# Optimization experiments

Measured on AMD Instinct MI355X. Metric: run time of the kernel, lower is better.

Reference implementation:

```python
import jax, jax.numpy as jnp
import numpy as np

EMBED = 768
HEADS = 6
HEAD_DIM = 256
SEQ = 128
BATCH = 512
EPS = 1e-5


def _layernorm(x, g, b):
    mu = jnp.mean(x, axis=-1, keepdims=True)
    var = jnp.mean(jnp.square(x - mu), axis=-1, keepdims=True)
    return (x - mu) * jax.lax.rsqrt(var + EPS) * g + b


def setup_inputs() -> dict:
    key = jax.random.key(0)
    ks = jax.random.split(key, 10)
    s_in = 1.0 / np.sqrt(EMBED)
    s_cat = 1.0 / np.sqrt(HEADS * HEAD_DIM)
    s_ff = 1.0 / np.sqrt(4 * EMBED)
    return {
        "x": jax.random.normal(ks[0], (BATCH, SEQ, EMBED), jnp.float32),
        # per-head projections (bias=False), stacked over heads: [H, E, D]
        "Wq": jax.random.uniform(ks[1], (HEADS, EMBED, HEAD_DIM), jnp.float32, -s_in, s_in),
        "Wk": jax.random.uniform(ks[2], (HEADS, EMBED, HEAD_DIM), jnp.float32, -s_in, s_in),
        "Wv": jax.random.uniform(ks[3], (HEADS, EMBED, HEAD_DIM), jnp.float32, -s_in, s_in),
        "Wo": jax.random.uniform(ks[4], (HEADS * HEAD_DIM, EMBED), jnp.float32, -s_cat, s_cat),
        "bo": jax.random.uniform(ks[5], (EMBED,), jnp.float32, -s_cat, s_cat),
        "W1": jax.random.uniform(ks[6], (EMBED, 4 * EMBED), jnp.float32, -s_in, s_in),
        "b1": jax.random.uniform(ks[7], (4 * EMBED,), jnp.float32, -s_in, s_in),
        "W2": jax.random.uniform(ks[8], (4 * EMBED, EMBED), jnp.float32, -s_ff, s_ff),
        "b2": jax.random.uniform(ks[9], (EMBED,), jnp.float32, -s_ff, s_ff),
        "g1": jnp.ones((EMBED,), jnp.float32),
        "be1": jnp.zeros((EMBED,), jnp.float32),
        "g2": jnp.ones((EMBED,), jnp.float32),
        "be2": jnp.zeros((EMBED,), jnp.float32),
    }


def reference(x, Wq, Wk, Wv, Wo, bo, W1, b1, W2, b2, g1, be1, g2, be2):
    B, T, E = x.shape
    h = _layernorm(x, g1, be1)
    # per-head projections: [B, H, T, D]
    q = jnp.einsum("bte,hed->bhtd", h, Wq)
    k = jnp.einsum("bte,hed->bhtd", h, Wk)
    v = jnp.einsum("bte,hed->bhtd", h, Wv)
    # NOTE: faithful to source — scale by embed_size**-0.5, not head_size**-0.5
    scores = jnp.einsum("bhtd,bhsd->bhts", q, k) * (E ** -0.5)
    causal = jnp.tril(jnp.ones((T, T), bool))
    scores = jnp.where(causal, scores, -jnp.inf)
    attn = jax.nn.softmax(scores, axis=-1)
    head_out = jnp.einsum("bhts,bhsd->bhtd", attn, v)
    # concat heads in order -> [B, T, H*D]
    cat = head_out.transpose(0, 2, 1, 3).reshape(B, T, HEADS * HEAD_DIM)
    attn_out = cat @ Wo + bo + x
    h2 = _layernorm(attn_out, g2, be2)
    mlp = jax.nn.relu(h2 @ W1 + b1) @ W2 + b2
    return mlp + attn_out
```

## Files before the change

kernel.cpp:

```cpp
#include <hip/hip_runtime.h>
#include <hip/hip_bf16.h>

#define BATCH 512
#define SEQ   128
#define EMB   768
#define NH    6
#define HDIM  256
#define CATD  1536
#define FFD   3072
#define NTOK  (BATCH*SEQ)
#define QKVLD 4608

typedef __attribute__((ext_vector_type(8))) short bfrag;
typedef __attribute__((ext_vector_type(4))) float f32x4;

__device__ __forceinline__ void gld_lds16(const void* g, void* l) {
  __builtin_amdgcn_global_load_lds(
      (const __attribute__((address_space(1))) unsigned int*)g,
      (__attribute__((address_space(3))) unsigned int*)l, 16, 0, 0);
}

__device__ __forceinline__ unsigned short f2bfu(float f) {
  union { __hip_bfloat16 h; unsigned short u; } c;
  c.h = __float2bfloat16(f);
  return c.u;
}

__device__ __forceinline__ void transpose64(const float* in, int C,
                                            __hip_bfloat16* out, int R,
                                            int r0, int c0) {
  __shared__ float tile[64][65];
  const int tx = threadIdx.x & 63;
  const int ty = threadIdx.x >> 6;
#pragma unroll
  for (int i = 0; i < 16; ++i) {
    const int r = ty + i * 4;
    tile[r][tx] = in[(size_t)(r0 + r) * C + c0 + tx];
  }
  __syncthreads();
#pragma unroll
  for (int i = 0; i < 16; ++i) {
    const int cc = ty + i * 4;
    out[(size_t)(c0 + cc) * R + r0 + tx] = __float2bfloat16(tile[tx][cc]);
  }
}

__global__ __launch_bounds__(256) void transpose_cast(const float* __restrict__ in,
                                                      __hip_bfloat16* __restrict__ out,
                                                      int R, int C) {
  transpose64(in, C, out, R, blockIdx.y * 64, blockIdx.x * 64);
}

__global__ __launch_bounds__(256) void repack_qkv(const float* __restrict__ Wq,
                                                  const float* __restrict__ Wk,
                                                  const float* __restrict__ Wv,
                                                  __hip_bfloat16* __restrict__ out) {
  const int z = blockIdx.z, m = z / NH, h = z % NH;
  const float* in = (m == 0 ? Wq : (m == 1 ? Wk : Wv)) + (size_t)h * EMB * HDIM;
  __hip_bfloat16* o = out + (size_t)(m * CATD + h * HDIM) * EMB;
  transpose64(in, HDIM, o, EMB, blockIdx.y * 64, blockIdx.x * 64);
}

__global__ __launch_bounds__(256) void ln_k(const float* __restrict__ src,
                                            const float* __restrict__ gam,
                                            const float* __restrict__ bet,
                                            __hip_bfloat16* __restrict__ dst) {
  const int row = blockIdx.x * 4 + (threadIdx.x >> 6);
  const int l = threadIdx.x & 63;
  const float* x = src + (size_t)row * EMB;
  float4 v[3];
#pragma unroll
  for (int j = 0; j < 3; ++j) v[j] = *(const float4*)(x + j * 256 + l * 4);
  float s = 0.f, ss = 0.f;
#pragma unroll
  for (int j = 0; j < 3; ++j) {
    s  += v[j].x + v[j].y + v[j].z + v[j].w;
    ss += v[j].x * v[j].x + v[j].y * v[j].y + v[j].z * v[j].z + v[j].w * v[j].w;
  }
#pragma unroll
  for (int d = 1; d < 64; d <<= 1) { s += __shfl_xor(s, d, 64); ss += __shfl_xor(ss, d, 64); }
  const float mu = s * (1.f / EMB);
  const float var = ss * (1.f / EMB) - mu * mu;
  const float rs = rsqrtf(var + 1e-5f);
#pragma unroll
  for (int j = 0; j < 3; ++j) {
    float4 g4 = *(const float4*)(gam + j * 256 + l * 4);
    float4 b4 = *(const float4*)(bet + j * 256 + l * 4);
    ushort4 o;
    o.x = f2bfu((v[j].x - mu) * rs * g4.x + b4.x);
    o.y = f2bfu((v[j].y - mu) * rs * g4.y + b4.y);
    o.z = f2bfu((v[j].z - mu) * rs * g4.z + b4.z);
    o.w = f2bfu((v[j].w - mu) * rs * g4.w + b4.w);
    *(ushort4*)((unsigned short*)dst + (size_t)row * EMB + j * 256 + l * 4) = o;
  }
}

#define PHASE(S, MH) do {                                                    \
    bfrag af[4], bv[4];                                                      \
    const char* Ab = cbuf + ((S)*16 + wm*8 + (MH)*4) * 1024 + l * 16;        \
    const char* Bb = cbuf + 32768 + ((S)*16 + wn*4) * 1024 + l * 16;         \
    _Pragma("unroll")                                                        \
    for (int i = 0; i < 4; ++i) af[i] = *(const bfrag*)(Ab + i * 1024);      \
    _Pragma("unroll")                                                        \
    for (int n = 0; n < 4; ++n) bv[n] = *(const bfrag*)(Bb + n * 1024);      \
    __builtin_amdgcn_s_setprio(1);                                          \
    _Pragma("unroll")                                                        \
    for (int i = 0; i < 4; ++i)                                              \
      _Pragma("unroll")                                                      \
      for (int n = 0; n < 4; ++n)                                            \
        acc[(MH)*4 + i][n] = __builtin_amdgcn_mfma_f32_16x16x32_bf16(        \
            af[i], bv[n], acc[(MH)*4 + i][n], 0, 0, 0);                      \
    __builtin_amdgcn_s_setprio(0);                                          \
  } while (0)

#define PH_END                                                \
  asm volatile("s_waitcnt lgkmcnt(0)" ::: "memory");          \
  asm volatile("s_barrier" ::: "memory")

#define STG(p, koff, dstoff) gld_lds16((p) + (koff), lds + (dstoff))

template <int MODE>
__global__ __launch_bounds__(512, 2)
void gemm_k(const __hip_bfloat16* __restrict__ A, const __hip_bfloat16* __restrict__ Bt,
            void* __restrict__ Cout, const float* __restrict__ bias,
            const float* __restrict__ res, int M, int N, int K) {
  __shared__ char lds[131072];
  const int tid = threadIdx.x;
  const int w = tid >> 6, l = tid & 63;
  const int l15 = l & 15, lq = l >> 4;
  const int wm = w >> 2, wn = w & 3;

  const int nwg = gridDim.x * gridDim.y;
  const int orig = blockIdx.y * gridDim.x + blockIdx.x;
  const int cpx = nwg >> 3;
  const int sw = (orig & 7) * cpx + (orig >> 3);
  const int n0 = (sw % gridDim.x) * 256;
  const int m0 = (sw / gridDim.x) * 256;

  const unsigned short* Au = (const unsigned short*)A;
  const unsigned short* Bu = (const unsigned short*)Bt;
  const unsigned short* pA_lo = Au + (size_t)(m0 + w * 16 + l15) * K + lq * 8;
  const unsigned short* pA_hi = Au + (size_t)(m0 + 128 + w * 16 + l15) * K + lq * 8;
  const unsigned short* pB_lo = Bu + (size_t)(n0 + w * 16 + l15) * K + lq * 8;
  const unsigned short* pB_hi = Bu + (size_t)(n0 + 128 + w * 16 + l15) * K + lq * 8;

  f32x4 acc[8][4];
#pragma unroll
  for (int i = 0; i < 8; ++i)
#pragma unroll
    for (int n = 0; n < 4; ++n) acc[i][n] = {0.f, 0.f, 0.f, 0.f};

  const int kIters = K >> 6;

  STG(pA_lo, 0,  (0 + w) * 1024);
  STG(pA_hi, 0,  (8 + w) * 1024);
  STG(pB_lo, 0,  32768 + (0 + w) * 1024);
  STG(pB_hi, 0,  32768 + (8 + w) * 1024);
  STG(pA_lo, 32, (16 + w) * 1024);
  STG(pA_hi, 32, (24 + w) * 1024);
  STG(pB_lo, 32, 32768 + (16 + w) * 1024);
  STG(pB_hi, 32, 32768 + (24 + w) * 1024);
  STG(pA_lo, 64, 65536 + (0 + w) * 1024);
  STG(pA_hi, 64, 65536 + (8 + w) * 1024);
  STG(pB_lo, 64, 65536 + 32768 + (0 + w) * 1024);
  STG(pB_hi, 64, 65536 + 32768 + (8 + w) * 1024);

  for (int kt = 0; kt < kIters; ++kt) {
    const int cOff = (kt & 1) * 65536;
    const int nOff = cOff ^ 65536;
    const char* cbuf = lds + cOff;
    const bool pre1 = (kt + 1 < kIters);
    const bool pre2 = (kt + 2 < kIters);
    const int k1 = (kt + 1) * 64 + 32;
    const int k2 = (kt + 2) * 64;

    if (pre1) {
      STG(pA_lo, k1, nOff + (16 + w) * 1024);
      STG(pB_lo, k1, nOff + 32768 + (16 + w) * 1024);
      asm volatile("s_waitcnt vmcnt(6)" ::: "memory");
    } else {
      asm volatile("s_waitcnt vmcnt(0)" ::: "memory");
    }
    asm volatile("s_barrier" ::: "memory");
    PHASE(0, 0);
    PH_END;
    if (pre1) {
      STG(pA_hi, k1, nOff + (24 + w) * 1024);
      STG(pB_hi, k1, nOff + 32768 + (24 + w) * 1024);
    }
    PHASE(0, 1);
    PH_END;
    if (pre2) {
      STG(pA_lo, k2, cOff + (0 + w) * 1024);
      STG(pB_lo, k2, cOff + 32768 + (0 + w) * 1024);
    }
    PHASE(1, 0);
    PH_END;
    if (pre2) {
      STG(pA_hi, k2, cOff + (8 + w) * 1024);
      STG(pB_hi, k2, cOff + 32768 + (8 + w) * 1024);
    }
    PHASE(1, 1);
    PH_END;
  }

  float bcol[4];
  if (MODE != 0) {
#pragma unroll
    for (int n = 0; n < 4; ++n) bcol[n] = bias[n0 + wn * 64 + n * 16 + l15];
  }
  if (MODE == 1) {
#pragma unroll
    for (int q = 0; q < 4; ++q) {
      if (q) __syncthreads();
      if (wm == (q >> 1)) {
#pragma unroll
        for (int i2 = 0; i2 < 4; ++i2)
#pragma unroll
          for (int n = 0; n < 4; ++n)
#pragma unroll
            for (int r = 0; r < 4; ++r) {
              const int lrow = i2 * 16 + lq * 4 + r;
              const int col = wn * 64 + n * 16 + l15;
              ((float*)lds)[lrow * 260 + col] = acc[(q & 1) * 4 + i2][n][r] + bcol[n];
            }
      }
      __syncthreads();
#pragma unroll
      for (int rep = 0; rep < 8; ++rep) {
        const int row = rep * 8 + (tid >> 6);
        const int colf = (tid & 63) * 4;
        float4 v = *(const float4*)((const float*)lds + row * 260 + colf);
        const size_t gidx = (size_t)(m0 + q * 64 + row) * N + n0 + colf;
        const float4 rv = *(const float4*)(res + gidx);
        v.x += rv.x; v.y += rv.y; v.z += rv.z; v.w += rv.w;
        *(float4*)((float*)Cout + gidx) = v;
      }
    }
  } else {
#pragma unroll
    for (int p = 0; p < 2; ++p) {
      if (p) __syncthreads();
      if (wm == p) {
#pragma unroll
        for (int i = 0; i < 8; ++i)
#pragma unroll
          for (int n = 0; n < 4; ++n)
#pragma unroll
            for (int r = 0; r < 4; ++r) {
              const int lrow = i * 16 + lq * 4 + r;
              const int col = wn * 64 + n * 16 + l15;
              float v = acc[i][n][r];
              if (MODE == 2) v = fmaxf(v + bcol[n], 0.f);
              ((unsigned short*)lds)[lrow * 264 + col] = f2bfu(v);
            }
      }
      __syncthreads();
#pragma unroll
      for (int rep = 0; rep < 8; ++rep) {
        const int row = rep * 16 + (tid >> 5);
        const int colc = (tid & 31) * 8;
        const uint4 v = *(const uint4*)((const unsigned short*)lds + row * 264 + colc);
        *(uint4*)((__hip_bfloat16*)Cout + (size_t)(m0 + p * 128 + row) * N + n0 + colc) = v;
      }
    }
  }
}

#undef PHASE
#undef PH_END
#undef STG

__global__ __launch_bounds__(256, 2)
void attn_k(const __hip_bfloat16* __restrict__ qkv, __hip_bfloat16* __restrict__ cat) {
  __shared__ char sm[17408 + 34816 + 2048];
  char* stage = sm;
  unsigned short* P = (unsigned short*)(sm + 17408);
  float* redm = (float*)(sm + 17408 + 34816);
  float* reds = redm + 256;

  const int tid = threadIdx.x;
  const int w = tid >> 6, l = tid & 63;
  const int l15 = l & 15, lq = l >> 4;
  const int wm = w >> 1, wn = w & 1;
  const int bh = blockIdx.x, b = bh / NH, h = bh % NH;
  const unsigned short* qkvu = (const unsigned short*)qkv;
  const size_t tokbase = (size_t)b * SEQ;
  const int qcol = h * HDIM, kcol = CATD + h * HDIM, vcol = 2 * CATD + h * HDIM;

  f32x4 acc[4][4];
#pragma unroll
  for (int i = 0; i < 4; ++i)
#pragma unroll
    for (int j = 0; j < 4; ++j) acc[i][j] = {0.f, 0.f, 0.f, 0.f};

  for (int d0 = 0; d0 < HDIM; d0 += 32) {
#pragma unroll
    for (int i = 0; i < 4; ++i) {
      const int ch = w * 4 + i;
      const int rowloc = (ch & 7) * 16 + l15;
      const int colbase = (ch < 8 ? qcol : kcol) + d0 + lq * 8;
      gld_lds16(qkvu + (tokbase + rowloc) * QKVLD + colbase, stage + ch * 1024);
    }
    __syncthreads();
    bfrag af[4], bf[4];
#pragma unroll
    for (int i = 0; i < 4; ++i) {
      af[i] = *(const bfrag*)(stage + ((wm * 4 + i) * 64 + l) * 16);
      bf[i] = *(const bfrag*)(stage + 8192 + ((wn * 4 + i) * 64 + l) * 16);
    }
#pragma unroll
    for (int i = 0; i < 4; ++i)
#pragma unroll
      for (int j = 0; j < 4; ++j)
        acc[i][j] = __builtin_amdgcn_mfma_f32_16x16x32_bf16(af[i], bf[j], acc[i][j], 0, 0, 0);
    __syncthreads();
  }

  const float scl = 0.03608439182435161f;
  const int rowb = wm * 64 + lq * 4;
  const int colb = wn * 64 + l15;
  float rmax[4][4];
#pragma unroll
  for (int i = 0; i < 4; ++i)
#pragma unroll
    for (int r = 0; r < 4; ++r) {
      const int row = rowb + i * 16 + r;
      float m = -__builtin_inff();
#pragma unroll
      for (int j = 0; j < 4; ++j) {
        const int col = colb + j * 16;
        float sv = acc[i][j][r] * scl;
        if (col > row) sv = -__builtin_inff();
        acc[i][j][r] = sv;
        m = fmaxf(m, sv);
      }
#pragma unroll
      for (int d = 1; d < 16; d <<= 1) m = fmaxf(m, __shfl_xor(m, d, 64));
      rmax[i][r] = m;
    }
  if (l15 == 0) {
#pragma unroll
    for (int i = 0; i < 4; ++i)
#pragma unroll
      for (int r = 0; r < 4; ++r)
        redm[wn * 128 + rowb + i * 16 + r] = rmax[i][r];
  }
  __syncthreads();
  float rsum[4][4];
#pragma unroll
  for (int i = 0; i < 4; ++i)
#pragma unroll
    for (int r = 0; r < 4; ++r) {
      const int row = rowb + i * 16 + r;
      const float mfin = fmaxf(redm[row], redm[128 + row]);
      float sacc = 0.f;
#pragma unroll
      for (int j = 0; j < 4; ++j) {
        float p = __expf(acc[i][j][r] - mfin);
        acc[i][j][r] = p;
        sacc += p;
      }
#pragma unroll
      for (int d = 1; d < 16; d <<= 1) sacc += __shfl_xor(sacc, d, 64);
      rsum[i][r] = sacc;
    }
  if (l15 == 0) {
#pragma unroll
    for (int i = 0; i < 4; ++i)
#pragma unroll
      for (int r = 0; r < 4; ++r)
        reds[wn * 128 + rowb + i * 16 + r] = rsum[i][r];
  }
#pragma unroll
  for (int i = 0; i < 4; ++i)
#pragma unroll
    for (int j = 0; j < 4; ++j)
#pragma unroll
      for (int r = 0; r < 4; ++r)
        P[(rowb + i * 16 + r) * 136 + colb + j * 16] = f2bfu(acc[i][j][r]);
  __syncthreads();

  float invs[4][4];
#pragma unroll
  for (int i = 0; i < 4; ++i)
#pragma unroll
    for (int r = 0; r < 4; ++r) {
      const int row = rowb + i * 16 + r;
      invs[i][r] = 1.f / (reds[row] + reds[128 + row]);
    }

  unsigned short* Vt = (unsigned short*)stage;
  for (int dt = 0; dt < 4; ++dt) {
#pragma unroll
    for (int p4 = 0; p4 < 4; ++p4) {
      const int slot = tid + p4 * 256;
      const int s = slot >> 3, dblk = slot & 7;
      uint4 val = *(const uint4*)(qkvu + (tokbase + s) * QKVLD + vcol + dt * 64 + dblk * 8);
      union { uint4 v; unsigned short u[8]; } uu; uu.v = val;
#pragma unroll
      for (int jj = 0; jj < 8; ++jj) Vt[(dblk * 8 + jj) * 136 + s] = uu.u[jj];
    }
    __syncthreads();
    f32x4 oacc[4][2];
#pragma unroll
    for (int i = 0; i < 4; ++i) { oacc[i][0] = {0.f,0.f,0.f,0.f}; oacc[i][1] = {0.f,0.f,0.f,0.f}; }
#pragma unroll
    for (int ks = 0; ks < 4; ++ks) {
      bfrag pf[4], vf[2];
#pragma unroll
      for (int i = 0; i < 4; ++i)
        pf[i] = *(const bfrag*)((char*)P + ((wm * 64 + i * 16 + l15) * 136 + ks * 32 + lq * 8) * 2);
#pragma unroll
      for (int j = 0; j < 2; ++j)
        vf[j] = *(const bfrag*)((char*)Vt + (((wn * 2 + j) * 16 + l15) * 136 + ks * 32 + lq * 8) * 2);
#pragma unroll
      for (int i = 0; i < 4; ++i)
#pragma unroll
        for (int j = 0; j < 2; ++j)
          oacc[i][j] = __builtin_amdgcn_mfma_f32_16x16x32_bf16(pf[i], vf[j], oacc[i][j], 0, 0, 0);
    }
#pragma unroll
    for (int i = 0; i < 4; ++i)
#pragma unroll
      for (int j = 0; j < 2; ++j)
#pragma unroll
        for (int r = 0; r < 4; ++r) {
          const int trow = rowb + i * 16 + r;
          const int dcol = dt * 64 + wn * 32 + j * 16 + l15;
          cat[(tokbase + trow) * CATD + h * HDIM + dcol] =
              __float2bfloat16(oacc[i][j][r] * invs[i][r]);
        }
    __syncthreads();
  }
}

extern "C" void kernel_launch(void* const* d_in, const int* in_sizes, int n_in,
                              void* d_out, int out_size, void* d_ws, size_t ws_size,
                              hipStream_t stream) {
  const float* x   = (const float*)d_in[0];
  const float* Wq  = (const float*)d_in[1];
  const float* Wk  = (const float*)d_in[2];
  const float* Wv  = (const float*)d_in[3];
  const float* Wo  = (const float*)d_in[4];
  const float* bo  = (const float*)d_in[5];
  const float* W1  = (const float*)d_in[6];
  const float* b1  = (const float*)d_in[7];
  const float* W2  = (const float*)d_in[8];
  const float* b2  = (const float*)d_in[9];
  const float* g1  = (const float*)d_in[10];
  const float* be1 = (const float*)d_in[11];
  const float* g2  = (const float*)d_in[12];
  const float* be2 = (const float*)d_in[13];
  float* out = (float*)d_out;

  const size_t wbytes = (size_t)QKVLD * EMB * 2 + (size_t)EMB * CATD * 2 +
                        (size_t)FFD * EMB * 2 + (size_t)EMB * FFD * 2;
  int nc = 1;
  while (nc < 16 &&
         wbytes + (size_t)(NTOK / nc) * (9216 + 3072 + 3072) + 4096 > ws_size)
    nc <<= 1;
  const int Mc = NTOK / nc;
  const int Bc = BATCH / nc;

  char* ws = (char*)d_ws;
  size_t off = 0;
  auto alloc = [&](size_t bytes) {
    char* p = ws + off;
    off += (bytes + 255) & ~(size_t)255;
    return p;
  };
  __hip_bfloat16* Wqkv_t = (__hip_bfloat16*)alloc((size_t)QKVLD * EMB * 2);
  __hip_bfloat16* Wo_t   = (__hip_bfloat16*)alloc((size_t)EMB * CATD * 2);
  __hip_bfloat16* W1_t   = (__hip_bfloat16*)alloc((size_t)FFD * EMB * 2);
  __hip_bfloat16* W2_t   = (__hip_bfloat16*)alloc((size_t)EMB * FFD * 2);
  char* R1 = (char*)alloc((size_t)Mc * 9216);
  char* R2 = (char*)alloc((size_t)Mc * 3072);
  char* R3 = (char*)alloc((size_t)Mc * 3072);

  repack_qkv<<<dim3(HDIM / 64, EMB / 64, 18), 256, 0, stream>>>(Wq, Wk, Wv, Wqkv_t);
  transpose_cast<<<dim3(EMB / 64, CATD / 64), 256, 0, stream>>>(Wo, Wo_t, CATD, EMB);
  transpose_cast<<<dim3(FFD / 64, EMB / 64), 256, 0, stream>>>(W1, W1_t, EMB, FFD);
  transpose_cast<<<dim3(EMB / 64, FFD / 64), 256, 0, stream>>>(W2, W2_t, FFD, EMB);

  for (int c = 0; c < nc; ++c) {
    const float* xc   = x + (size_t)c * Mc * EMB;
    float*       outc = out + (size_t)c * Mc * EMB;
    __hip_bfloat16* hbuf   = (__hip_bfloat16*)R3;
    __hip_bfloat16* qkv    = (__hip_bfloat16*)R1;
    __hip_bfloat16* cat    = (__hip_bfloat16*)R2;
    float*          attn_o = (float*)R3;
    __hip_bfloat16* h2     = (__hip_bfloat16*)R2;
    __hip_bfloat16* mlp1   = (__hip_bfloat16*)R1;

    ln_k<<<Mc / 4, 256, 0, stream>>>(xc, g1, be1, hbuf);
    gemm_k<0><<<dim3(QKVLD / 256, Mc / 256), 512, 0, stream>>>(
        hbuf, Wqkv_t, qkv, nullptr, nullptr, Mc, QKVLD, EMB);
    attn_k<<<Bc * NH, 256, 0, stream>>>(qkv, cat);
    gemm_k<1><<<dim3(EMB / 256, Mc / 256), 512, 0, stream>>>(
        cat, Wo_t, attn_o, bo, xc, Mc, EMB, CATD);
    ln_k<<<Mc / 4, 256, 0, stream>>>(attn_o, g2, be2, h2);
    gemm_k<2><<<dim3(FFD / 256, Mc / 256), 512, 0, stream>>>(
        h2, W1_t, mlp1, b1, nullptr, Mc, FFD, EMB);
    gemm_k<1><<<dim3(EMB / 256, Mc / 256), 512, 0, stream>>>(
        mlp1, W2_t, outc, b2, attn_o, Mc, EMB, FFD);
  }
}
```

Measured before the change: 2.429 ms.

## Reorder GEMM main loop to issue LDS reads before global prefetch

Each GEMM phase is split into an LDS fragment-read step and an MFMA step. The LDS reads are now issued before the next global-to-LDS prefetch, and barriers wrap the MFMA block. The vmcnt wait moves from the start of each k-iteration to its last phase, with a new wait and barrier after the prologue. The aim is to overlap LDS read latency with the global load issue and to tighten the synchronisation schedule, at the cost of one extra barrier per phase.

Result: no change. 2.384 ms (-1.8%).

```diff
diff --git a/kernel.cpp b/kernel.cpp
--- a/kernel.cpp
+++ b/kernel.cpp
@@ -95,27 +95,29 @@
   }
 }
 
-#define PHASE(S, MH) do {                                                    \
+#define PH_DS(S, MH)                                                         \
     bfrag af[4], bv[4];                                                      \
-    const char* Ab = cbuf + ((S)*16 + wm*8 + (MH)*4) * 1024 + l * 16;        \
-    const char* Bb = cbuf + 32768 + ((S)*16 + wn*4) * 1024 + l * 16;         \
-    _Pragma("unroll")                                                        \
-    for (int i = 0; i < 4; ++i) af[i] = *(const bfrag*)(Ab + i * 1024);      \
-    _Pragma("unroll")                                                        \
-    for (int n = 0; n < 4; ++n) bv[n] = *(const bfrag*)(Bb + n * 1024);      \
-    __builtin_amdgcn_s_setprio(1);                                          \
+    {                                                                        \
+      const char* Ab = cbuf + ((S)*16 + wm*8 + (MH)*4) * 1024 + l * 16;      \
+      const char* Bb = cbuf + 32768 + ((S)*16 + wn*4) * 1024 + l * 16;       \
+      _Pragma("unroll")                                                      \
+      for (int i = 0; i < 4; ++i) af[i] = *(const bfrag*)(Ab + i * 1024);    \
+      _Pragma("unroll")                                                      \
+      for (int n = 0; n < 4; ++n) bv[n] = *(const bfrag*)(Bb + n * 1024);    \
+    }
+
+#define PH_MFMA(MH)                                                          \
+    __builtin_amdgcn_s_barrier();                                            \
+    asm volatile("s_waitcnt lgkmcnt(0)" ::: "memory");                       \
+    __builtin_amdgcn_s_setprio(1);                                           \
     _Pragma("unroll")                                                        \
     for (int i = 0; i < 4; ++i)                                              \
       _Pragma("unroll")                                                      \
       for (int n = 0; n < 4; ++n)                                            \
         acc[(MH)*4 + i][n] = __builtin_amdgcn_mfma_f32_16x16x32_bf16(        \
             af[i], bv[n], acc[(MH)*4 + i][n], 0, 0, 0);                      \
-    __builtin_amdgcn_s_setprio(0);                                          \
-  } while (0)
-
-#define PH_END                                                \
-  asm volatile("s_waitcnt lgkmcnt(0)" ::: "memory");          \
-  asm volatile("s_barrier" ::: "memory")
+    __builtin_amdgcn_s_setprio(0);                                           \
+    __builtin_amdgcn_s_barrier();
 
 #define STG(p, koff, dstoff) gld_lds16((p) + (koff), lds + (dstoff))
 
@@ -164,6 +166,8 @@
   STG(pA_hi, 64, 65536 + (8 + w) * 1024);
   STG(pB_lo, 64, 65536 + 32768 + (0 + w) * 1024);
   STG(pB_hi, 64, 65536 + 32768 + (8 + w) * 1024);
+  asm volatile("s_waitcnt vmcnt(4)" ::: "memory");
+  __builtin_amdgcn_s_barrier();
 
   for (int kt = 0; kt < kIters; ++kt) {
     const int cOff = (kt & 1) * 65536;
@@ -174,34 +178,41 @@
     const int k1 = (kt + 1) * 64 + 32;
     const int k2 = (kt + 2) * 64;
 
-    if (pre1) {
-      STG(pA_lo, k1, nOff + (16 + w) * 1024);
-      STG(pB_lo, k1, nOff + 32768 + (16 + w) * 1024);
-      asm volatile("s_waitcnt vmcnt(6)" ::: "memory");
-    } else {
-      asm volatile("s_waitcnt vmcnt(0)" ::: "memory");
-    }
-    asm volatile("s_barrier" ::: "memory");
-    PHASE(0, 0);
-    PH_END;
-    if (pre1) {
-      STG(pA_hi, k1, nOff + (24 + w) * 1024);
-      STG(pB_hi, k1, nOff + 32768 + (24 + w) * 1024);
-    }
-    PHASE(0, 1);
-    PH_END;
-    if (pre2) {
-      STG(pA_lo, k2, cOff + (0 + w) * 1024);
-      STG(pB_lo, k2, cOff + 32768 + (0 + w) * 1024);
-    }
-    PHASE(1, 0);
-    PH_END;
-    if (pre2) {
-      STG(pA_hi, k2, cOff + (8 + w) * 1024);
-      STG(pB_hi, k2, cOff + 32768 + (8 + w) * 1024);
-    }
-    PHASE(1, 1);
-    PH_END;
+    {
+      PH_DS(0, 0);
+      if (pre1) {
+        STG(pA_lo, k1, nOff + (16 + w) * 1024);
+        STG(pB_lo, k1, nOff + 32768 + (16 + w) * 1024);
+      }
+      PH_MFMA(0);
+    }
+    {
+      PH_DS(0, 1);
+      if (pre1) {
+        STG(pA_hi, k1, nOff + (24 + w) * 1024);
+        STG(pB_hi, k1, nOff + 32768 + (24 + w) * 1024);
+      }
+      PH_MFMA(1);
+    }
+    {
+      PH_DS(1, 0);
+      if (pre2) {
+        STG(pA_lo, k2, cOff + (0 + w) * 1024);
+        STG(pB_lo, k2, cOff + 32768 + (0 + w) * 1024);
+      }
+      PH_MFMA(0);
+    }
+    {
+      PH_DS(1, 1);
+      if (pre2) {
+        STG(pA_hi, k2, cOff + (8 + w) * 1024);
+        STG(pB_hi, k2, cOff + 32768 + (8 + w) * 1024);
+        asm volatile("s_waitcnt vmcnt(4)" ::: "memory");
+      } else {
+        asm volatile("s_waitcnt vmcnt(0)" ::: "memory");
+      }
+      PH_MFMA(1);
+    }
   }
 
   float bcol[4];
@@ -267,8 +278,8 @@
   }
 }
 
-#undef PHASE
-#undef PH_END
+#undef PH_DS
+#undef PH_MFMA
 #undef STG
 
 __global__ __launch_bounds__(256, 2)
```
